# Kernel tuning notes

Hardware: AMD Instinct MI355X
Metric: run time of the kernel (lower is better)

## Reference

```python
import jax, jax.numpy as jnp
import numpy as np

B, S, D, H, V = 4, 1024, 2048, 16, 32000
LAYERS, DFF, HID, NSENT, NLAB = 2, 8192, 100, 3, 3
HD = D // H
LN2 = 0.6931471805599453


def _ln(x, g, b):
    m = jnp.mean(x, axis=-1, keepdims=True)
    v = jnp.mean((x - m) ** 2, axis=-1, keepdims=True)
    return (x - m) * jax.lax.rsqrt(v + 1e-5) * g + b


def setup_inputs():
    key = jax.random.key(0)
    ks = jax.random.split(key, 12)
    s = 0.02
    return dict(
        input_ids=jax.random.randint(ks[0], (B, S), 0, V),
        attention_mask=jnp.ones((B, S), dtype=jnp.int32),
        sentiment=jax.random.normal(ks[1], (B, NSENT), dtype=jnp.float32),
        perplexity=jax.random.uniform(ks[2], (B,), dtype=jnp.float32) + 1.0,
        emb=jax.random.normal(ks[3], (V, D), dtype=jnp.float32) * s,
        ln1_g=jnp.ones((LAYERS, D)), ln1_b=jnp.zeros((LAYERS, D)),
        qkv_w=jax.random.normal(ks[4], (LAYERS, D, 3 * D), dtype=jnp.float32) * s,
        wo_w=jax.random.normal(ks[5], (LAYERS, D, D), dtype=jnp.float32) * s,
        ln2_g=jnp.ones((LAYERS, D)), ln2_b=jnp.zeros((LAYERS, D)),
        w1=jax.random.normal(ks[6], (LAYERS, D, DFF), dtype=jnp.float32) * s,
        w2=jax.random.normal(ks[7], (LAYERS, DFF, D), dtype=jnp.float32) * s,
        lnf_g=jnp.ones((D,)), lnf_b=jnp.zeros((D,)),
        head_w=jax.random.normal(ks[8], (D, V), dtype=jnp.float32) * s,
        red_w=jax.random.normal(ks[9], (D, HID), dtype=jnp.float32) * s,
        red_b=jnp.zeros((HID,)),
        cls_w=jax.random.normal(ks[10], (HID + NSENT + 2, NLAB), dtype=jnp.float32) * s,
        cls_b=jnp.zeros((NLAB,)),
    )


def _lm(input_ids, attention_mask, emb, ln1_g, ln1_b, qkv_w, wo_w, ln2_g, ln2_b, w1, w2, lnf_g, lnf_b, head_w):
    x = emb[input_ids]  # [B,S,D]
    amask = attention_mask.astype(jnp.float32)
    causal = jnp.tril(jnp.ones((S, S), dtype=bool))
    bias = jnp.where(causal[None, None, :, :] & (amask[:, None, None, :] > 0), 0.0, -1e9)
    for l in range(LAYERS):
        h = _ln(x, ln1_g[l], ln1_b[l])
        qkv = h @ qkv_w[l]  # [B,S,3D]
        q, k, v = [t.reshape(B, S, H, HD) for t in jnp.split(qkv, 3, axis=-1)]
        scores = jnp.einsum('bqhd,bkhd->bhqk', q, k) / np.float32(np.sqrt(HD)) + bias
        attn = jax.nn.softmax(scores, axis=-1)
        o = jnp.einsum('bhqk,bkhd->bqhd', attn, v).reshape(B, S, D)
        x = x + o @ wo_w[l]
        h = _ln(x, ln2_g[l], ln2_b[l])
        x = x + jax.nn.gelu(h @ w1[l]) @ w2[l]
    h = _ln(x, lnf_g, lnf_b)
    logits = h @ head_w  # [B,S,V]
    return h, logits


def reference(input_ids, attention_mask, sentiment, perplexity, emb, ln1_g, ln1_b, qkv_w, wo_w, ln2_g, ln2_b, w1, w2, lnf_g, lnf_b, head_w, red_w, red_b, cls_w, cls_b):
    h, logits = _lm(input_ids, attention_mask, emb, ln1_g, ln1_b, qkv_w, wo_w,
                    ln2_g, ln2_b, w1, w2, lnf_g, lnf_b, head_w)
    amask = attention_mask.astype(jnp.float32)
    pooled = jnp.mean(h, axis=1)  # mean over seq -> [B,D]
    # probs = softmax(logits).detach(); gather own token prob; -log2(p)
    lg = jax.lax.stop_gradient(logits)
    logZ = jax.scipy.special.logsumexp(lg, axis=-1)  # [B,S]
    tok_logit = jnp.take_along_axis(lg, input_ids[..., None], axis=-1)[..., 0]
    subword_surp = -(tok_logit - logZ) / LN2 * amask
    mean_surprisal = subword_surp.sum(axis=1) / amask.sum(axis=1)  # [B]
    r = jax.nn.leaky_relu(pooled @ red_w + red_b)  # torch intent: LeakyReLU after reducer
    feats = jnp.concatenate([r, sentiment, perplexity[:, None], mean_surprisal[:, None]], axis=1)
    return feats @ cls_w + cls_b  # [B, NLAB]
```

## Files before the change

### kernel.cpp

```cpp
#include <hip/hip_runtime.h>

typedef unsigned short u16;
typedef unsigned char u8;
typedef __bf16 bf16x8 __attribute__((ext_vector_type(8)));
typedef float f32x4 __attribute__((ext_vector_type(4)));

__device__ __forceinline__ u16 f2bf(float f){
  unsigned u = __float_as_uint(f);
  unsigned r = u + 0x7FFFu + ((u >> 16) & 1u);
  return (u16)(r >> 16);
}
__device__ __forceinline__ float bf2f(u16 v){ return __uint_as_float(((unsigned)v) << 16); }

__device__ __forceinline__ u8 f2fp8(float f){
  unsigned u = __float_as_uint(f);
  u8 s = (u >> 24) & 0x80;
  float a = __uint_as_float(u & 0x7FFFFFFF);
  if (!(a < 464.f)) return s | 0x7E;
  unsigned eu = u & 0x7F800000u;
  unsigned cb = eu + (20u << 23);
  const unsigned cmin = 141u << 23;
  float c = __uint_as_float(cb > cmin ? cb : cmin);
  float q = (a + c) - c;
  if (q > 448.f) return s | 0x7E;
  if (q == 0.f) return s;
  unsigned uq = __float_as_uint(q);
  int eq = (int)(uq >> 23) - 127;
  if (eq < -6){
    int mq = (int)(q * 512.f);
    return s | (u8)mq;
  }
  return s | (u8)(((eq + 7) << 3) | ((uq >> 20) & 7));
}

__device__ __forceinline__ void gload16(const void* g, void* l){
  __builtin_amdgcn_global_load_lds(
      (const __attribute__((address_space(1))) unsigned int*)g,
      (__attribute__((address_space(3))) unsigned int*)l, 16, 0, 0);
}

__global__ __launch_bounds__(256) void transp_k(const float* __restrict__ in, u16* __restrict__ out, int K, int N)
{
  __shared__ float tl[64][65];
  const int n0 = blockIdx.x * 64, k0 = blockIdx.y * 64;
  const int t = threadIdx.x;
  const int r = t >> 4, c4 = t & 15;
#pragma unroll
  for (int i = 0; i < 4; ++i){
    float4 v = *(const float4*)(in + (size_t)(k0 + r + i*16) * N + n0 + c4*4);
    tl[r + i*16][c4*4 + 0] = v.x; tl[r + i*16][c4*4 + 1] = v.y;
    tl[r + i*16][c4*4 + 2] = v.z; tl[r + i*16][c4*4 + 3] = v.w;
  }
  __syncthreads();
#pragma unroll
  for (int i = 0; i < 4; ++i){
    const int n = r + i*16;
    ushort4 o;
    o.x = f2bf(tl[c4*4 + 0][n]); o.y = f2bf(tl[c4*4 + 1][n]);
    o.z = f2bf(tl[c4*4 + 2][n]); o.w = f2bf(tl[c4*4 + 3][n]);
    *(ushort4*)(out + (size_t)(n0 + n) * K + k0 + c4*4) = o;
  }
}

__global__ __launch_bounds__(256) void transp8_k(const float* __restrict__ in, u8* __restrict__ out, int K, int N)
{
  __shared__ float tl[64][65];
  const int n0 = blockIdx.x * 64, k0 = blockIdx.y * 64;
  const int t = threadIdx.x;
  const int r = t >> 4, c4 = t & 15;
#pragma unroll
  for (int i = 0; i < 4; ++i){
    float4 v = *(const float4*)(in + (size_t)(k0 + r + i*16) * N + n0 + c4*4);
    tl[r + i*16][c4*4 + 0] = v.x; tl[r + i*16][c4*4 + 1] = v.y;
    tl[r + i*16][c4*4 + 2] = v.z; tl[r + i*16][c4*4 + 3] = v.w;
  }
  __syncthreads();
#pragma unroll
  for (int i = 0; i < 4; ++i){
    const int n = r + i*16;
    uchar4 o;
    o.x = f2fp8(tl[c4*4 + 0][n] * 16.f); o.y = f2fp8(tl[c4*4 + 1][n] * 16.f);
    o.z = f2fp8(tl[c4*4 + 2][n] * 16.f); o.w = f2fp8(tl[c4*4 + 3][n] * 16.f);
    const int ng = n0 + n;
    const int k = k0 + c4 * 4;
    const int key = (ng >> 2) & 3;
    const size_t addr = (size_t)ng * K + (k & ~31) + ((((k >> 3) & 3) ^ key) << 3) + (k & 7);
    *(uchar4*)(out + addr) = o;
  }
}

__global__ __launch_bounds__(256) void embed_k(const int* __restrict__ ids, const float* __restrict__ emb, float* __restrict__ x)
{
  const int row = blockIdx.x;
  const int c = blockIdx.y * 256 + threadIdx.x;
  x[(size_t)row * 2048 + c] = emb[(size_t)ids[row] * 2048 + c];
}

template<int OM>
__global__ __launch_bounds__(256) void ln_k(const float* __restrict__ x, const float* __restrict__ gw,
                                            const float* __restrict__ bw, u16* __restrict__ o, u8* __restrict__ o8)
{
  const int row = blockIdx.x, t = threadIdx.x;
  const int lane = t & 63, wid = t >> 6;
  const float4* xr = (const float4*)(x + (size_t)row * 2048);
  float4 v1 = xr[t], v2 = xr[t + 256];
  float s1 = v1.x + v1.y + v1.z + v1.w + v2.x + v2.y + v2.z + v2.w;
  float s2 = v1.x*v1.x + v1.y*v1.y + v1.z*v1.z + v1.w*v1.w
           + v2.x*v2.x + v2.y*v2.y + v2.z*v2.z + v2.w*v2.w;
#pragma unroll
  for (int off = 32; off >= 1; off >>= 1){ s1 += __shfl_down(s1, off); s2 += __shfl_down(s2, off); }
  __shared__ float rb[2][4];
  __shared__ float mv[2];
  if (lane == 0){ rb[0][wid] = s1; rb[1][wid] = s2; }
  __syncthreads();
  if (t == 0){
    float a = rb[0][0] + rb[0][1] + rb[0][2] + rb[0][3];
    float q = rb[1][0] + rb[1][1] + rb[1][2] + rb[1][3];
    float mean = a * (1.f/2048.f);
    float var  = q * (1.f/2048.f) - mean*mean;
    mv[0] = mean; mv[1] = rsqrtf(var + 1e-5f);
  }
  __syncthreads();
  const float mean = mv[0], rstd = mv[1];
  const float4* g4 = (const float4*)gw;
  const float4* b4 = (const float4*)bw;
  float4 ga = g4[t], ba = b4[t], gb = g4[t + 256], bb2 = b4[t + 256];
  float n1x = (v1.x - mean)*rstd*ga.x + ba.x;
  float n1y = (v1.y - mean)*rstd*ga.y + ba.y;
  float n1z = (v1.z - mean)*rstd*ga.z + ba.z;
  float n1w = (v1.w - mean)*rstd*ga.w + ba.w;
  float n2x = (v2.x - mean)*rstd*gb.x + bb2.x;
  float n2y = (v2.y - mean)*rstd*gb.y + bb2.y;
  float n2z = (v2.z - mean)*rstd*gb.z + bb2.z;
  float n2w = (v2.w - mean)*rstd*gb.w + bb2.w;
  if constexpr (OM != 1){
    ushort4 o1, o2;
    o1.x = f2bf(n1x); o1.y = f2bf(n1y); o1.z = f2bf(n1z); o1.w = f2bf(n1w);
    o2.x = f2bf(n2x); o2.y = f2bf(n2y); o2.z = f2bf(n2z); o2.w = f2bf(n2w);
    ((ushort4*)(o + (size_t)row * 2048))[t] = o1;
    ((ushort4*)(o + (size_t)row * 2048))[t + 256] = o2;
  }
  if constexpr (OM != 0){
    uchar4 q1, q2;
    q1.x = f2fp8(n1x); q1.y = f2fp8(n1y); q1.z = f2fp8(n1z); q1.w = f2fp8(n1w);
    q2.x = f2fp8(n2x); q2.y = f2fp8(n2y); q2.z = f2fp8(n2z); q2.w = f2fp8(n2w);
    const int key = (row >> 2) & 3;
    const int k1 = t * 4;
    const int k2 = 1024 + t * 4;
    const int a1 = (k1 & ~31) + ((((k1 >> 3) & 3) ^ key) << 3) + (k1 & 7);
    const int a2 = (k2 & ~31) + ((((k2 >> 3) & 3) ^ key) << 3) + (k2 & 7);
    *(uchar4*)(o8 + (size_t)row * 2048 + a1) = q1;
    *(uchar4*)(o8 + (size_t)row * 2048 + a2) = q2;
  }
}

enum { M_QKV = 0, M_RES = 1, M_GELU = 2, M_LSE = 3 };

template<int MODE, int BM>
__global__ __launch_bounds__(512, 2) void gemm2_k(
    const u16* __restrict__ A, const u16* __restrict__ BT,
    int N, int K, int MB,
    u16* __restrict__ outb, float* __restrict__ outf)
{
  constexpr int BK  = 32;
  constexpr int ASZ = BM * BK;
  constexpr int BSZ = 256 * BK;
  constexpr int BUF = ASZ + BSZ;
  constexpr int NFR = BM / 32;
  __shared__ u16 lds[3 * BUF];

  const int tid  = threadIdx.x;
  const int wv   = tid >> 6, lane = tid & 63;
  const int wr   = wv >> 2,  wc   = wv & 3;
  const int lg   = lane >> 4, lr  = lane & 15;

  const int nwg = gridDim.x;
  const int bid = blockIdx.x;
  const int swz = ((nwg & 7) == 0) ? ((bid & 7) * (nwg >> 3) + (bid >> 3)) : bid;
  const int bm = swz % MB, bn = swz / MB;
  const int m0 = bm * BM, n0 = bn * 256;

  const int ll = lane >> 3;
  const int cc = lane & 7;
  const int lc = cc ^ ll;
  const int gr = (ll << 1) + (lc >> 2);
  const int gk = (lc & 3) << 3;

  const u16* gA = A  + (size_t)m0 * K + gk;
  const u16* gB = BT + (size_t)n0 * K + gk;

  f32x4 acc[NFR][4];
#pragma unroll
  for (int i = 0; i < NFR; ++i)
#pragma unroll
    for (int j = 0; j < 4; ++j)
#pragma unroll
      for (int r = 0; r < 4; ++r) acc[i][j][r] = 0.f;

  const int nt = K >> 5;

  auto STAGE = [&](int bi, int kt){
    char* bA = (char*)lds + (size_t)bi * BUF * 2;
    char* bB = bA + ASZ * 2;
    const size_t ko = (size_t)kt * 32;
    gload16(gA + (size_t)(wv * 16 + gr) * K + ko, bA + wv * 1024);
    gload16(gB + (size_t)((wv    ) * 16 + gr) * K + ko, bB + (wv    ) * 1024);
    gload16(gB + (size_t)((wv + 8) * 16 + gr) * K + ko, bB + (wv + 8) * 1024);
  };

  STAGE(0, 0);
  STAGE(1, 1);

  for (int t = 0; t < nt; ++t){
    if (t + 1 < nt) asm volatile("s_waitcnt vmcnt(3) lgkmcnt(0)" ::: "memory");
    else            asm volatile("s_waitcnt vmcnt(0) lgkmcnt(0)" ::: "memory");
    __builtin_amdgcn_s_barrier();
    if (t + 2 < nt) STAGE((t + 2) % 3, t + 2);

    const char* bA = (const char*)lds + (size_t)(t % 3) * BUF * 2;
    const char* bB = bA + ASZ * 2;
    bf16x8 af[NFR], bq[4];
#pragma unroll
    for (int i = 0; i < NFR; ++i){
      const int ra = wr * (BM / 2) + i * 16 + lr;
      const int p = ra >> 1;
      const int slot = (((ra & 1) << 2) | lg) ^ (p & 7);
      af[i] = *(const bf16x8*)(bA + p * 128 + slot * 16);
    }
#pragma unroll
    for (int j = 0; j < 4; ++j){
      const int rb = wc * 64 + j * 16 + lr;
      const int p = rb >> 1;
      const int slot = (((rb & 1) << 2) | lg) ^ (p & 7);
      bq[j] = *(const bf16x8*)(bB + p * 128 + slot * 16);
    }
    __builtin_amdgcn_s_setprio(1);
#pragma unroll
    for (int i = 0; i < NFR; ++i)
#pragma unroll
      for (int j = 0; j < 4; ++j)
        acc[i][j] = __builtin_amdgcn_mfma_f32_16x16x32_bf16(af[i], bq[j], acc[i][j], 0, 0, 0);
    __builtin_amdgcn_s_setprio(0);
  }

#pragma unroll
  for (int i = 0; i < NFR; ++i){
#pragma unroll
    for (int r = 0; r < 4; ++r){
      const int row = m0 + wr * (BM / 2) + i * 16 + lg * 4 + r;
#pragma unroll
      for (int j = 0; j < 4; ++j){
        const int col = n0 + wc * 64 + j * 16 + lr;
        const float v = acc[i][j][r];
        if constexpr (MODE == M_RES){
          float* pp = outf + (size_t)row * N + col;
          *pp += v;
        } else if constexpr (MODE == M_GELU){
          float u = 0.7978845608028654f * (v + 0.044715f * v * v * v);
          u = fminf(fmaxf(u, -15.f), 15.f);
          const float ex = __expf(2.f * u);
          const float th = (ex - 1.f) / (ex + 1.f);
          outb[(size_t)row * N + col] = f2bf(0.5f * v * (1.f + th));
        }
      }
    }
  }
}

template<int MODE>
__global__ __launch_bounds__(512, 2) void gemm6_k(
    const u16* __restrict__ A, const u16* __restrict__ BT,
    int N, int K, int MB,
    u16* __restrict__ outb, float* __restrict__ outf, u16* __restrict__ vtout)
{
  __shared__ u16 lds[65536];

  const int tid  = threadIdx.x;
  const int wv   = tid >> 6, lane = tid & 63;
  const int wr   = wv >> 2,  wc   = wv & 3;
  const int lg   = lane >> 4, lr  = lane & 15;

  const int nwg = gridDim.x;
  const int bid = blockIdx.x;
  const int swz = ((nwg & 7) == 0) ? ((bid & 7) * (nwg >> 3) + (bid >> 3)) : bid;
  const int bm = swz % MB, bn = swz / MB;
  const int m0 = bm * 256, n0 = bn * 256;

  const int ll = lane >> 3;
  const int cc = lane & 7;
  const int lc = cc ^ ll;
  const int gr = (ll << 1) + (lc >> 2);
  const int gk = (lc & 3) << 3;

  const u16* gA = A  + (size_t)m0 * K + gk;
  const u16* gB = BT + (size_t)n0 * K + gk;

  f32x4 acc[8][4];
#pragma unroll
  for (int i = 0; i < 8; ++i)
#pragma unroll
    for (int j = 0; j < 4; ++j)
#pragma unroll
      for (int r = 0; r < 4; ++r) acc[i][j][r] = 0.f;

  const int nt = K >> 6;

  auto RB = [&](int tt, int kh, int bsel) -> char* {
    return (char*)lds + (((tt & 1) << 16) | (kh << 15) | (bsel << 14));
  };
  auto STG = [&](const u16* gsrc, int tt, int kh, int bsel){
    char* dst = RB(tt, kh, bsel);
    const size_t ko = (size_t)tt * 64 + kh * 32;
    gload16(gsrc + (size_t)((wv    ) * 16 + gr) * K + ko, dst + (wv    ) * 1024);
    gload16(gsrc + (size_t)((wv + 8) * 16 + gr) * K + ko, dst + (wv + 8) * 1024);
  };
  auto FRG = [&](int tt, int kh, int bsel, int row) -> bf16x8 {
    const int p = row >> 1;
    const int slot = (((row & 1) << 2) | lg) ^ (p & 7);
    return *(const bf16x8*)(RB(tt, kh, bsel) + p * 128 + slot * 16);
  };

  STG(gA, 0, 0, 0); STG(gB, 0, 0, 1);
  STG(gA, 0, 1, 0); STG(gB, 0, 1, 1);
  STG(gA, 1, 0, 0); STG(gB, 1, 0, 1);
  asm volatile("s_waitcnt vmcnt(4)" ::: "memory");
  __builtin_amdgcn_s_barrier();

  for (int u = 0; u < nt; ++u){
    bf16x8 bq[4], aa[4];
#pragma unroll
    for (int j = 0; j < 4; ++j) bq[j] = FRG(u, 0, 1, wc * 64 + j * 16 + lr);
#pragma unroll
    for (int i = 0; i < 4; ++i) aa[i] = FRG(u, 0, 0, wr * 128 + i * 16 + lr);
    if (u + 1 < nt) STG(gA, u + 1, 1, 0);
    __builtin_amdgcn_s_barrier();
    asm volatile("s_waitcnt lgkmcnt(0)" ::: "memory");
    __builtin_amdgcn_s_setprio(1);
#pragma unroll
    for (int i = 0; i < 4; ++i)
#pragma unroll
      for (int j = 0; j < 4; ++j)
        acc[i][j] = __builtin_amdgcn_mfma_f32_16x16x32_bf16(aa[i], bq[j], acc[i][j], 0, 0, 0);
    __builtin_amdgcn_s_setprio(0);
    __builtin_amdgcn_s_barrier();

    bf16x8 ab[4];
#pragma unroll
    for (int i = 0; i < 4; ++i) ab[i] = FRG(u, 0, 0, wr * 128 + (4 + i) * 16 + lr);
    if (u + 1 < nt) STG(gB, u + 1, 1, 1);
    __builtin_amdgcn_s_barrier();
    asm volatile("s_waitcnt lgkmcnt(0)" ::: "memory");
    __builtin_amdgcn_s_setprio(1);
#pragma unroll
    for (int i = 0; i < 4; ++i)
#pragma unroll
      for (int j = 0; j < 4; ++j)
        acc[4 + i][j] = __builtin_amdgcn_mfma_f32_16x16x32_bf16(ab[i], bq[j], acc[4 + i][j], 0, 0, 0);
    __builtin_amdgcn_s_setprio(0);
    __builtin_amdgcn_s_barrier();

    bf16x8 bq2[4], ac[4];
#pragma unroll
    for (int j = 0; j < 4; ++j) bq2[j] = FRG(u, 1, 1, wc * 64 + j * 16 + lr);
#pragma unroll
    for (int i = 0; i < 4; ++i) ac[i] = FRG(u, 1, 0, wr * 128 + i * 16 + lr);
    if (u + 2 < nt) STG(gA, u + 2, 0, 0);
    __builtin_amdgcn_s_barrier();
    asm volatile("s_waitcnt lgkmcnt(0)" ::: "memory");
    __builtin_amdgcn_s_setprio(1);
#pragma unroll
    for (int i = 0; i < 4; ++i)
#pragma unroll
      for (int j = 0; j < 4; ++j)
        acc[i][j] = __builtin_amdgcn_mfma_f32_16x16x32_bf16(ac[i], bq2[j], acc[i][j], 0, 0, 0);
    __builtin_amdgcn_s_setprio(0);
    __builtin_amdgcn_s_barrier();

    bf16x8 ad[4];
#pragma unroll
    for (int i = 0; i < 4; ++i) ad[i] = FRG(u, 1, 0, wr * 128 + (4 + i) * 16 + lr);
    if (u + 2 < nt) STG(gB, u + 2, 0, 1);
    if (u + 2 < nt)      asm volatile("s_waitcnt vmcnt(4)" ::: "memory");
    else if (u + 1 < nt) asm volatile("s_waitcnt vmcnt(0)" ::: "memory");
    __builtin_amdgcn_s_barrier();
    asm volatile("s_waitcnt lgkmcnt(0)" ::: "memory");
    __builtin_amdgcn_s_setprio(1);
#pragma unroll
    for (int i = 0; i < 4; ++i)
#pragma unroll
      for (int j = 0; j < 4; ++j)
        acc[4 + i][j] = __builtin_amdgcn_mfma_f32_16x16x32_bf16(ad[i], bq2[j], acc[4 + i][j], 0, 0, 0);
    __builtin_amdgcn_s_setprio(0);
    __builtin_amdgcn_s_barrier();
  }

#pragma unroll
  for (int i = 0; i < 8; ++i){
    if constexpr (MODE == M_QKV){
#pragma unroll
      for (int j = 0; j < 4; ++j){
        const int colb = n0 + wc * 64 + j * 16;
        if (colb < 4096){
#pragma unroll
          for (int r = 0; r < 4; ++r){
            const int row = m0 + wr * 128 + i * 16 + lg * 4 + r;
            outb[(size_t)row * 6144 + colb + lr] = f2bf(acc[i][j][r]);
          }
        } else {
          const int srow = m0 + wr * 128 + i * 16 + lg * 4;
          const int b = srow >> 10, s = srow & 1023;
          int dd = colb + lr - 4096;
          const int hh = dd >> 7; dd &= 127;
          ushort4 o;
          o.x = f2bf(acc[i][j][0]); o.y = f2bf(acc[i][j][1]);
          o.z = f2bf(acc[i][j][2]); o.w = f2bf(acc[i][j][3]);
          *(ushort4*)(vtout + ((size_t)(b * 16 + hh) * 128 + dd) * 1024 + s) = o;
        }
      }
    } else {
#pragma unroll
      for (int r = 0; r < 4; ++r){
        const int row = m0 + wr * 128 + i * 16 + lg * 4 + r;
#pragma unroll
        for (int j = 0; j < 4; ++j){
          const int col = n0 + wc * 64 + j * 16 + lr;
          const float v = acc[i][j][r];
          if constexpr (MODE == M_RES){
            float* pp = outf + (size_t)row * N + col;
            *pp += v;
          } else {
            float u2 = 0.7978845608028654f * (v + 0.044715f * v * v * v);
            u2 = fminf(fmaxf(u2, -15.f), 15.f);
            const float ex = __expf(2.f * u2);
            const float th = (ex - 1.f) / (ex + 1.f);
            outb[(size_t)row * N + col] = f2bf(0.5f * v * (1.f + th));
          }
        }
      }
    }
  }
}

template<int MODE>
__global__ __launch_bounds__(512, 2) void gemm8_k(
    const u8* __restrict__ A8, const u8* __restrict__ B8,
    int N, int K, int MB,
    u16* __restrict__ outb,
    float* __restrict__ partial, float* __restrict__ tokl,
    const int* __restrict__ ids)
{
  __shared__ u8 lds8[2 * 16384];

  const int tid  = threadIdx.x;
  const int wv   = tid >> 6, lane = tid & 63;
  const int wr   = wv >> 2,  wc   = wv & 3;
  const int lg   = lane >> 4, lr  = lane & 15;

  const int nwg = gridDim.x;
  const int bid = blockIdx.x;
  const int swz = ((nwg & 7) == 0) ? ((bid & 7) * (nwg >> 3) + (bid >> 3)) : bid;
  const int bm = swz % MB, bn = swz / MB;
  const int m0 = bm * 256, n0 = bn * 256;

  const int sr = lane >> 1, sh = (lane & 1) << 4;
  const u8* gA = A8 + (size_t)(m0 + wv * 32 + sr) * K + sh;
  const u8* gB = B8 + (size_t)(n0 + wv * 32 + sr) * K + sh;

  f32x4 acc[8][4];
#pragma unroll
  for (int i = 0; i < 8; ++i)
#pragma unroll
    for (int j = 0; j < 4; ++j)
#pragma unroll
      for (int r = 0; r < 4; ++r) acc[i][j][r] = 0.f;

  const int nt = K >> 5;

  auto STAGE = [&](int bi, int kt){
    u8* base = lds8 + bi * 16384;
    gload16(gA + (size_t)kt * 32, base + wv * 1024);
    gload16(gB + (size_t)kt * 32, base + 8192 + wv * 1024);
  };

  auto FR8 = [&](const u8* base, int r) -> long {
    const int p = r >> 2;
    const int g = ((r & 3) << 2) | (lg ^ (p & 3));
    return *(const long*)(base + p * 128 + g * 8);
  };

  STAGE(0, 0);
  STAGE(1, 1);

  for (int t = 0; t < nt; ++t){
    if (t + 1 < nt) asm volatile("s_waitcnt vmcnt(2)" ::: "memory");
    else            asm volatile("s_waitcnt vmcnt(0)" ::: "memory");
    __builtin_amdgcn_s_barrier();

    const u8* bA = lds8 + (t & 1) * 16384;
    const u8* bB = bA + 8192;
    long af[8], bq[4];
#pragma unroll
    for (int i = 0; i < 8; ++i) af[i] = FR8(bA, wr * 128 + i * 16 + lr);
#pragma unroll
    for (int j = 0; j < 4; ++j) bq[j] = FR8(bB, wc * 64 + j * 16 + lr);
    asm volatile("s_waitcnt lgkmcnt(0)" ::: "memory");
    __builtin_amdgcn_s_barrier();

    if (t + 2 < nt) STAGE(t & 1, t + 2);

    __builtin_amdgcn_s_setprio(1);
#pragma unroll
    for (int i = 0; i < 8; ++i)
#pragma unroll
      for (int j = 0; j < 4; ++j)
        acc[i][j] = __builtin_amdgcn_mfma_f32_16x16x32_fp8_fp8(af[i], bq[j], acc[i][j], 0, 0, 0);
    __builtin_amdgcn_s_setprio(0);
  }

#pragma unroll
  for (int i = 0; i < 8; ++i){
    if constexpr (MODE == M_LSE){
#pragma unroll
      for (int r = 0; r < 4; ++r){
        const int row = m0 + wr * 128 + i * 16 + lg * 4 + r;
        const int id = ids[row];
        float esum = 0.f;
#pragma unroll
        for (int j = 0; j < 4; ++j){
          const int col = n0 + wc * 64 + j * 16 + lr;
          const float v = acc[i][j][r] * 0.0625f;
          if (col == id) tokl[row] = v;
          esum += __expf(v);
        }
#pragma unroll
        for (int off = 8; off >= 1; off >>= 1) esum += __shfl_xor(esum, off);
        if (lr == 0) partial[(size_t)row * 500 + bn * 4 + wc] = esum;
      }
    } else {
#pragma unroll
      for (int r = 0; r < 4; ++r){
        const int row = m0 + wr * 128 + i * 16 + lg * 4 + r;
#pragma unroll
        for (int j = 0; j < 4; ++j){
          const int col = n0 + wc * 64 + j * 16 + lr;
          const float v = acc[i][j][r] * 0.0625f;
          float u = 0.7978845608028654f * (v + 0.044715f * v * v * v);
          u = fminf(fmaxf(u, -15.f), 15.f);
          const float ex = __expf(2.f * u);
          const float th = (ex - 1.f) / (ex + 1.f);
          outb[(size_t)row * N + col] = f2bf(0.5f * v * (1.f + th));
        }
      }
    }
  }
}

__global__ __launch_bounds__(64) void attn_k(const u16* __restrict__ qkv, const u16* __restrict__ vT, u16* __restrict__ o16)
{
  __shared__ u16 P[16 * 40];
  const int bid = blockIdx.x;
  const int qt = bid & 63, bh = bid >> 6;
  const int h = bh & 15, b = bh >> 4;
  const int lane = threadIdx.x, lg = lane >> 4, lr = lane & 15;
  const int q0 = qt << 4;
  const u16* qrow  = qkv + (size_t)(b * 1024 + q0 + lr) * 6144 + h * 128;
  const u16* krow  = qkv + (size_t)(b * 1024 + lr) * 6144 + 2048 + h * 128;
  const u16* vbase = vT + (size_t)(b * 16 + h) * 128 * 1024;

  bf16x8 qf[4];
#pragma unroll
  for (int c = 0; c < 4; ++c) qf[c] = *(const bf16x8*)(qrow + c * 32 + lg * 8);

  float m[4], l[4];
  f32x4 oacc[8];
#pragma unroll
  for (int r = 0; r < 4; ++r){ m[r] = -1e30f; l[r] = 0.f; }
#pragma unroll
  for (int f = 0; f < 8; ++f)
#pragma unroll
    for (int r = 0; r < 4; ++r) oacc[f][r] = 0.f;

  const float scale = 0.08838834764831845f;
  const int nk2 = (qt >> 1) + 1;
  for (int k2 = 0; k2 < nk2; ++k2){
    float e[2][4];
    float rmax[4];
#pragma unroll
    for (int r = 0; r < 4; ++r) rmax[r] = -1e30f;
#pragma unroll
    for (int hh = 0; hh < 2; ++hh){
      const int kt = k2 * 2 + hh;
      if (kt <= qt){
        f32x4 s;
#pragma unroll
        for (int r = 0; r < 4; ++r) s[r] = 0.f;
#pragma unroll
        for (int c = 0; c < 4; ++c){
          bf16x8 kf = *(const bf16x8*)(krow + (size_t)(kt * 16) * 6144 + c * 32 + lg * 8);
          s = __builtin_amdgcn_mfma_f32_16x16x32_bf16(qf[c], kf, s, 0, 0, 0);
        }
#pragma unroll
        for (int r = 0; r < 4; ++r){
          float sv = s[r] * scale;
          if (kt * 16 + lr > q0 + lg * 4 + r) sv = -1e30f;
          e[hh][r] = sv;
          rmax[r] = fmaxf(rmax[r], sv);
        }
      } else {
#pragma unroll
        for (int r = 0; r < 4; ++r) e[hh][r] = -1e30f;
      }
    }
#pragma unroll
    for (int off = 8; off >= 1; off >>= 1)
#pragma unroll
      for (int r = 0; r < 4; ++r) rmax[r] = fmaxf(rmax[r], __shfl_xor(rmax[r], off));
    float corr[4], rsum[4];
#pragma unroll
    for (int r = 0; r < 4; ++r){
      const float mn = fmaxf(m[r], rmax[r]);
      corr[r] = __expf(m[r] - mn);
      m[r] = mn;
      const float e0 = __expf(e[0][r] - mn);
      const float e1 = __expf(e[1][r] - mn);
      e[0][r] = e0; e[1][r] = e1;
      rsum[r] = e0 + e1;
    }
#pragma unroll
    for (int off = 8; off >= 1; off >>= 1)
#pragma unroll
      for (int r = 0; r < 4; ++r) rsum[r] += __shfl_xor(rsum[r], off);
#pragma unroll
    for (int r = 0; r < 4; ++r) l[r] = l[r] * corr[r] + rsum[r];
#pragma unroll
    for (int hh = 0; hh < 2; ++hh)
#pragma unroll
      for (int r = 0; r < 4; ++r)
        P[(lg * 4 + r) * 40 + hh * 16 + lr] = f2bf(e[hh][r]);
#pragma unroll
    for (int f = 0; f < 8; ++f)
#pragma unroll
      for (int r = 0; r < 4; ++r) oacc[f][r] = oacc[f][r] * corr[r];
    __syncthreads();
    const bf16x8 pa = *(const bf16x8*)((const u16*)P + lr * 40 + lg * 8);
#pragma unroll
    for (int f = 0; f < 8; ++f){
      bf16x8 vb = *(const bf16x8*)(vbase + (size_t)(f * 16 + lr) * 1024 + k2 * 32 + lg * 8);
      oacc[f] = __builtin_amdgcn_mfma_f32_16x16x32_bf16(pa, vb, oacc[f], 0, 0, 0);
    }
    __syncthreads();
  }
  u16* orow = o16 + (size_t)(b * 1024 + q0 + lg * 4) * 2048 + h * 128;
#pragma unroll
  for (int r = 0; r < 4; ++r){
    const float linv = 1.0f / l[r];
#pragma unroll
    for (int f = 0; f < 8; ++f)
      orow[(size_t)r * 2048 + f * 16 + lr] = f2bf(oacc[f][r] * linv);
  }
}

__global__ __launch_bounds__(256) void lse_k(const float* __restrict__ partial, const float* __restrict__ tokl,
                                             const int* __restrict__ amask, float* __restrict__ surp)
{
  const int row = blockIdx.x, t = threadIdx.x, lane = t & 63, wid = t >> 6;
  float s = 0.f;
  if (t < 250) s = partial[(size_t)row * 500 + t] + partial[(size_t)row * 500 + t + 250];
#pragma unroll
  for (int off = 32; off >= 1; off >>= 1) s += __shfl_down(s, off);
  __shared__ float rb[4];
  if (lane == 0) rb[wid] = s;
  __syncthreads();
  if (t == 0){
    const float tot = rb[0] + rb[1] + rb[2] + rb[3];
    surp[row] = (logf(tot) - tokl[row]) * 1.4426950408889634f * (float)amask[row];
  }
}

__global__ __launch_bounds__(256) void pool_k(const u16* __restrict__ h16, float* __restrict__ pooled)
{
  const int d = blockIdx.x * 256 + threadIdx.x;
  const int b = blockIdx.y;
  const u16* p = h16 + (size_t)b * 1024 * 2048 + d;
  float a0 = 0.f, a1 = 0.f, a2 = 0.f, a3 = 0.f;
  for (int s = 0; s < 1024; s += 4){
    a0 += bf2f(p[(size_t)(s + 0) * 2048]);
    a1 += bf2f(p[(size_t)(s + 1) * 2048]);
    a2 += bf2f(p[(size_t)(s + 2) * 2048]);
    a3 += bf2f(p[(size_t)(s + 3) * 2048]);
  }
  pooled[b * 2048 + d] = (a0 + a1 + a2 + a3) * (1.f / 1024.f);
}

__global__ __launch_bounds__(256) void cls_k(const float* __restrict__ pooled, const float* __restrict__ surp,
                                             const int* __restrict__ amask, const float* __restrict__ sent,
                                             const float* __restrict__ ppl, const float* __restrict__ redw,
                                             const float* __restrict__ redb, const float* __restrict__ clsw,
                                             const float* __restrict__ clsb, float* __restrict__ out)
{
  const int b = blockIdx.x, t = threadIdx.x;
  const int lane = t & 63, wid = t >> 6;
  __shared__ float pl[2048];
  __shared__ float feats[112];
  __shared__ float rbuf[2][4];
#pragma unroll
  for (int i = 0; i < 8; ++i) pl[t + i * 256] = pooled[b * 2048 + t + i * 256];
  float ssum = 0.f, msum = 0.f;
#pragma unroll
  for (int i = 0; i < 4; ++i){
    const int s = t + i * 256;
    ssum += surp[b * 1024 + s];
    msum += (float)amask[b * 1024 + s];
  }
#pragma unroll
  for (int off = 32; off >= 1; off >>= 1){ ssum += __shfl_down(ssum, off); msum += __shfl_down(msum, off); }
  if (lane == 0){ rbuf[0][wid] = ssum; rbuf[1][wid] = msum; }
  __syncthreads();
  if (t == 0){
    float a = 0.f, c = 0.f;
    for (int i = 0; i < 4; ++i){ a += rbuf[0][i]; c += rbuf[1][i]; }
    feats[104] = a / c;
  }
  if (t >= 100 && t < 103) feats[t] = sent[b * 3 + (t - 100)];
  if (t == 103) feats[103] = ppl[b];
  if (t < 100){
    float a = redb[t];
    for (int d = 0; d < 2048; ++d) a += pl[d] * redw[d * 100 + t];
    feats[t] = (a > 0.f) ? a : 0.01f * a;
  }
  __syncthreads();
  if (t < 3){
    float a = clsb[t];
    for (int i = 0; i < 105; ++i) a += feats[i] * clsw[i * 3 + t];
    out[b * 3 + t] = a;
  }
}

extern "C" void kernel_launch(void* const* d_in, const int* in_sizes, int n_in,
                              void* d_out, int out_size, void* d_ws, size_t ws_size,
                              hipStream_t stream)
{
  (void)in_sizes; (void)n_in; (void)out_size; (void)ws_size;
  const int*   ids   = (const int*)d_in[0];
  const int*   amask = (const int*)d_in[1];
  const float* sent  = (const float*)d_in[2];
  const float* ppl   = (const float*)d_in[3];
  const float* emb   = (const float*)d_in[4];
  const float* ln1g  = (const float*)d_in[5];
  const float* ln1b  = (const float*)d_in[6];
  const float* qkvw  = (const float*)d_in[7];
  const float* wow   = (const float*)d_in[8];
  const float* ln2g  = (const float*)d_in[9];
  const float* ln2b  = (const float*)d_in[10];
  const float* w1    = (const float*)d_in[11];
  const float* w2    = (const float*)d_in[12];
  const float* lnfg  = (const float*)d_in[13];
  const float* lnfb  = (const float*)d_in[14];
  const float* headw = (const float*)d_in[15];
  const float* redw  = (const float*)d_in[16];
  const float* redb  = (const float*)d_in[17];
  const float* clsw  = (const float*)d_in[18];
  const float* clsb  = (const float*)d_in[19];
  float* out = (float*)d_out;

  char* p = (char*)d_ws;
  u16* wqkvT = (u16*)p; p += (size_t)2 * 6144 * 2048 * 2;
  u16* woT   = (u16*)p; p += (size_t)2 * 2048 * 2048 * 2;
  u8*  w18   = (u8*)p;  p += (size_t)2 * 8192 * 2048;
  u16* w2T   = (u16*)p; p += (size_t)2 * 2048 * 8192 * 2;
  u8*  wh8   = (u8*)p;  p += (size_t)32000 * 2048;
  float* xbuf = (float*)p; p += (size_t)4096 * 2048 * 4;
  u16* h16   = (u16*)p; p += (size_t)4096 * 2048 * 2;
  u8*  h8    = (u8*)p;  p += (size_t)4096 * 2048;
  u16* qkv16 = (u16*)p;
  u16* vT16  = (u16*)(p + (size_t)4096 * 6144 * 2);
  u16* ffn16 = (u16*)p;
  p += (size_t)4096 * 6144 * 2 + (size_t)4096 * 2048 * 2;
  u16* o16   = (u16*)p; p += (size_t)4096 * 2048 * 2;
  float* partial = (float*)p; p += (size_t)4096 * 500 * 4;
  float* tokl = (float*)p; p += (size_t)4096 * 4;
  float* surp = (float*)p; p += (size_t)4096 * 4;
  float* pooled = (float*)p; p += (size_t)4 * 2048 * 4;

  for (int l = 0; l < 2; ++l){
    transp_k<<<dim3(6144/64, 2048/64), 256, 0, stream>>>(qkvw + (size_t)l*2048*6144, wqkvT + (size_t)l*6144*2048, 2048, 6144);
    transp_k<<<dim3(2048/64, 2048/64), 256, 0, stream>>>(wow  + (size_t)l*2048*2048, woT   + (size_t)l*2048*2048, 2048, 2048);
    transp8_k<<<dim3(8192/64, 2048/64), 256, 0, stream>>>(w1   + (size_t)l*2048*8192, w18   + (size_t)l*8192*2048, 2048, 8192);
    transp_k<<<dim3(2048/64, 8192/64), 256, 0, stream>>>(w2   + (size_t)l*8192*2048, w2T   + (size_t)l*2048*8192, 8192, 2048);
  }
  transp8_k<<<dim3(32000/64, 2048/64), 256, 0, stream>>>(headw, wh8, 2048, 32000);

  embed_k<<<dim3(4096, 8), 256, 0, stream>>>(ids, emb, xbuf);

  for (int l = 0; l < 2; ++l){
    ln_k<0><<<4096, 256, 0, stream>>>(xbuf, ln1g + l*2048, ln1b + l*2048, h16, nullptr);
    gemm6_k<M_QKV><<<16*24, 512, 0, stream>>>(h16, wqkvT + (size_t)l*6144*2048, 6144, 2048, 16,
                                              qkv16, nullptr, vT16);
    attn_k<<<4096, 64, 0, stream>>>(qkv16, vT16, o16);
    gemm2_k<M_RES,128><<<32*8, 512, 0, stream>>>(o16, woT + (size_t)l*2048*2048, 2048, 2048, 32,
                                                 nullptr, xbuf);
    ln_k<1><<<4096, 256, 0, stream>>>(xbuf, ln2g + l*2048, ln2b + l*2048, nullptr, h8);
    gemm8_k<M_GELU><<<16*32, 512, 0, stream>>>(h8, w18 + (size_t)l*8192*2048, 8192, 2048, 16,
                                               ffn16, nullptr, nullptr, nullptr);
    gemm2_k<M_RES,128><<<32*8, 512, 0, stream>>>(ffn16, w2T + (size_t)l*2048*8192, 2048, 8192, 32,
                                                 nullptr, xbuf);
  }
  ln_k<2><<<4096, 256, 0, stream>>>(xbuf, lnfg, lnfb, h16, h8);
  gemm8_k<M_LSE><<<16*125, 512, 0, stream>>>(h8, wh8, 32000, 2048, 16,
                                             nullptr, partial, tokl, ids);
  lse_k<<<4096, 256, 0, stream>>>(partial, tokl, amask, surp);
  pool_k<<<dim3(8, 4), 256, 0, stream>>>(h16, pooled);
  cls_k<<<4, 256, 0, stream>>>(pooled, surp, amask, sent, ppl, redw, redb, clsw, clsb, out);
}
```

Measured before the change: 2.241 ms.

## Use scaled 16x16x128 f8f6f4 MFMA with 128-deep K tiles in fp8 GEMM

The fp8 GEMM (used for FFN up-projection and the LM head) switches from the 16x16x32 fp8 MFMA to the MI355 scaled 16x16x128 f8f6f4 MFMA with unit scales. Each K step now stages 128 bytes of depth through double-buffered LDS (128 KB total) and gathers 32-byte operand fragments per lane. This is meant to cut instruction count and use the higher fp8 matrix throughput of the newer instruction. In exchange, LDS use grows fourfold, which likely limits the kernel to one block per CU, and the fragment reads and register use increase.

```diff
diff --git a/kernel.cpp b/kernel.cpp
--- a/kernel.cpp
+++ b/kernel.cpp
@@ -4,6 +4,7 @@
 typedef unsigned char u8;
 typedef __bf16 bf16x8 __attribute__((ext_vector_type(8)));
 typedef float f32x4 __attribute__((ext_vector_type(4)));
+typedef int i32x8 __attribute__((ext_vector_type(8)));
 
 __device__ __forceinline__ u16 f2bf(float f){
   unsigned u = __float_as_uint(f);
@@ -442,14 +443,14 @@
 }
 
 template<int MODE>
-__global__ __launch_bounds__(512, 2) void gemm8_k(
+__global__ __launch_bounds__(512, 2) void gemm9_k(
     const u8* __restrict__ A8, const u8* __restrict__ B8,
     int N, int K, int MB,
     u16* __restrict__ outb,
     float* __restrict__ partial, float* __restrict__ tokl,
     const int* __restrict__ ids)
 {
-  __shared__ u8 lds8[2 * 16384];
+  __shared__ u8 lds8[2 * 65536];
 
   const int tid  = threadIdx.x;
   const int wv   = tid >> 6, lane = tid & 63;
@@ -474,35 +475,47 @@
 #pragma unroll
       for (int r = 0; r < 4; ++r) acc[i][j][r] = 0.f;
 
-  const int nt = K >> 5;
+  const int nt = K >> 7;
 
   auto STAGE = [&](int bi, int kt){
-    u8* base = lds8 + bi * 16384;
-    gload16(gA + (size_t)kt * 32, base + wv * 1024);
-    gload16(gB + (size_t)kt * 32, base + 8192 + wv * 1024);
+    u8* base = lds8 + bi * 65536;
+    const size_t ko = (size_t)kt * 128;
+#pragma unroll
+    for (int kb = 0; kb < 4; ++kb)
+      gload16(gA + ko + kb * 32, base + kb * 8192 + wv * 1024);
+#pragma unroll
+    for (int kb = 0; kb < 4; ++kb)
+      gload16(gB + ko + kb * 32, base + 32768 + kb * 8192 + wv * 1024);
   };
 
-  auto FR8 = [&](const u8* base, int r) -> long {
+  auto FRX = [&](const u8* opb, int r) -> i32x8 {
+    const u8* sub = opb + lg * 8192;
     const int p = r >> 2;
-    const int g = ((r & 3) << 2) | (lg ^ (p & 3));
-    return *(const long*)(base + p * 128 + g * 8);
+    i32x8 a;
+#pragma unroll
+    for (int c = 0; c < 4; ++c){
+      const long v = *(const long*)(sub + p * 128 + ((((r & 3) << 2) | (c ^ (p & 3)))) * 8);
+      a[2*c]   = (int)v;
+      a[2*c+1] = (int)(v >> 32);
+    }
+    return a;
   };
 
   STAGE(0, 0);
   STAGE(1, 1);
 
   for (int t = 0; t < nt; ++t){
-    if (t + 1 < nt) asm volatile("s_waitcnt vmcnt(2)" ::: "memory");
+    if (t + 1 < nt) asm volatile("s_waitcnt vmcnt(8)" ::: "memory");
     else            asm volatile("s_waitcnt vmcnt(0)" ::: "memory");
     __builtin_amdgcn_s_barrier();
 
-    const u8* bA = lds8 + (t & 1) * 16384;
-    const u8* bB = bA + 8192;
-    long af[8], bq[4];
-#pragma unroll
-    for (int i = 0; i < 8; ++i) af[i] = FR8(bA, wr * 128 + i * 16 + lr);
-#pragma unroll
-    for (int j = 0; j < 4; ++j) bq[j] = FR8(bB, wc * 64 + j * 16 + lr);
+    const u8* bA = lds8 + (t & 1) * 65536;
+    const u8* bB = bA + 32768;
+    i32x8 af[8], bq[4];
+#pragma unroll
+    for (int i = 0; i < 8; ++i) af[i] = FRX(bA, wr * 128 + i * 16 + lr);
+#pragma unroll
+    for (int j = 0; j < 4; ++j) bq[j] = FRX(bB, wc * 64 + j * 16 + lr);
     asm volatile("s_waitcnt lgkmcnt(0)" ::: "memory");
     __builtin_amdgcn_s_barrier();
 
@@ -513,7 +526,8 @@
     for (int i = 0; i < 8; ++i)
 #pragma unroll
       for (int j = 0; j < 4; ++j)
-        acc[i][j] = __builtin_amdgcn_mfma_f32_16x16x32_fp8_fp8(af[i], bq[j], acc[i][j], 0, 0, 0);
+        acc[i][j] = __builtin_amdgcn_mfma_scale_f32_16x16x128_f8f6f4(
+            af[i], bq[j], acc[i][j], 0, 0, 0, 0x7F7F7F7F, 0, 0x7F7F7F7F);
     __builtin_amdgcn_s_setprio(0);
   }
 
@@ -800,13 +814,13 @@
     gemm2_k<M_RES,128><<<32*8, 512, 0, stream>>>(o16, woT + (size_t)l*2048*2048, 2048, 2048, 32,
                                                  nullptr, xbuf);
     ln_k<1><<<4096, 256, 0, stream>>>(xbuf, ln2g + l*2048, ln2b + l*2048, nullptr, h8);
-    gemm8_k<M_GELU><<<16*32, 512, 0, stream>>>(h8, w18 + (size_t)l*8192*2048, 8192, 2048, 16,
+    gemm9_k<M_GELU><<<16*32, 512, 0, stream>>>(h8, w18 + (size_t)l*8192*2048, 8192, 2048, 16,
                                                ffn16, nullptr, nullptr, nullptr);
     gemm2_k<M_RES,128><<<32*8, 512, 0, stream>>>(ffn16, w2T + (size_t)l*2048*8192, 2048, 8192, 32,
                                                  nullptr, xbuf);
   }
   ln_k<2><<<4096, 256, 0, stream>>>(xbuf, lnfg, lnfb, h16, h8);
-  gemm8_k<M_LSE><<<16*125, 512, 0, stream>>>(h8, wh8, 32000, 2048, 16,
+  gemm9_k<M_LSE><<<16*125, 512, 0, stream>>>(h8, wh8, 32000, 2048, 16,
                                              nullptr, partial, tokl, ids);
   lse_k<<<4096, 256, 0, stream>>>(partial, tokl, amask, surp);
   pool_k<<<dim3(8, 4), 256, 0, stream>>>(h16, pooled);
```

After: 2.248 ms. Within noise of the previous version (+0.3%).
